# Optimization experiments

Measured on AMD Instinct MI355X. Metric: run time of the kernel, lower is better.

Reference implementation:

```python
import jax, jax.numpy as jnp
import numpy as np

WSZ = 16   # cfg.window_size
GD = 64    # cfg.group_dim


def setup_inputs() -> dict:
    key = jax.random.key(0)
    k1, k2, k3, k4 = jax.random.split(key, 4)
    B, T, D = 8, 8192, 1024
    z = jax.random.normal(k1, (B, T, D), jnp.float32)
    token_lens = jax.random.randint(k2, (B, T), 1, 9).astype(jnp.int32)
    W1 = jax.random.normal(k3, (D, GD), jnp.float32) / np.sqrt(D)
    W2 = jax.random.normal(k4, (GD, GD), jnp.float32) / np.sqrt(GD)
    return {"z": z, "token_lens": token_lens, "W1": W1, "W2": W2, "target_len": 6144}


def _choose_pairs(local_sim, budget):
    # local_sim: (W-1,) sims of adjacent edges inside one window.
    # Greedy non-overlapping matching in descending-sim order, up to `budget` pairs.
    Wn = local_sim.shape[0] + 1
    order = jnp.argsort(-local_sim)

    def step(state, e):
        used, mr, picked = state
        ok = (picked < budget) & (~used[e]) & (~used[e + 1])
        used = used.at[e].set(used[e] | ok)
        used = used.at[e + 1].set(used[e + 1] | ok)
        mr = mr.at[e + 1].set(mr[e + 1] | ok)
        return (used, mr, picked + ok.astype(jnp.int32)), None

    init = (jnp.zeros(Wn, bool), jnp.zeros(Wn, bool), jnp.int32(0))
    (_, mr, _), _ = jax.lax.scan(step, init, order)
    return mr  # (W,) True at j -> merge token j into j-1


def reference(z, token_lens, W1, W2, target_len):
    B, T, D = z.shape
    nwin = T // WSZ  # T chosen divisible by WSZ -> all windows full
    merges_needed = T - target_len
    base, extra = merges_needed // nwin, merges_needed % nwin
    budgets = jnp.minimum(base + (jnp.arange(nwin) < extra), WSZ // 2).astype(jnp.int32)

    # grouping MLP + cosine-style adjacent similarity
    g = jnp.maximum(z @ W1, 0.0) @ W2                         # (B,T,GD)
    g = g / (jnp.linalg.norm(g, axis=-1, keepdims=True) + 1e-8)
    sim = jnp.sum(g[:, :-1] * g[:, 1:], axis=-1)              # (B,T-1)
    # pad boundary edge slot, view per-window; keep only intra-window edges
    sim_pad = jnp.pad(sim, ((0, 0), (0, 1)), constant_values=-jnp.inf)
    local = sim_pad.reshape(B, nwin, WSZ)[:, :, : WSZ - 1]    # (B,nwin,W-1)

    pick = jax.vmap(jax.vmap(_choose_pairs, in_axes=(0, 0)), in_axes=(0, None))
    merge_right = pick(local, budgets).reshape(B, T)          # (B,T) bool
    keep = ~merge_right

    # pairs are disjoint -> sequential torch loop == parallel weighted merge
    w = token_lens.astype(z.dtype)
    absorb = merge_right[:, 1:]                               # token i absorbs i+1
    wi, wj = w[:, :-1, None], w[:, 1:, None]
    merged = (z[:, :-1] * wi + z[:, 1:] * wj) / (wi + wj)
    z2 = jnp.concatenate([jnp.where(absorb[:, :, None], merged, z[:, :-1]), z[:, -1:]], axis=1)
    l2 = jnp.concatenate(
        [jnp.where(absorb, token_lens[:, :-1] + token_lens[:, 1:], token_lens[:, :-1]),
         token_lens[:, -1:]], axis=1)

    # stable compaction: kept indices first (order preserved), truncate
    order = jnp.argsort(~keep, axis=1)[:, :target_len]        # jax sort is stable
    z_new = jnp.take_along_axis(z2, order[:, :, None], axis=1)
    lens_new = jnp.take_along_axis(l2, order, axis=1)
    starts_new = jnp.cumsum(lens_new, axis=1) - lens_new
    return z_new, lens_new, starts_new
```

## Files before the change

### kernel.cpp

```cpp
#include <hip/hip_runtime.h>

#define B_ 8
#define T_ 8192
#define D_ 1024
#define GD_ 64
#define WSZ_ 16
#define NWIN_ (T_ / WSZ_)
#define PL1_ (4 * 32 * 512)
#define PL2_ (4 * 2 * 512)

typedef __attribute__((ext_vector_type(8))) short short8v;
typedef __attribute__((ext_vector_type(4))) float f32x4;

__device__ __forceinline__ unsigned bf16rne(unsigned u) {
  return (u + 0x7FFFu + ((u >> 16) & 1u)) >> 16;
}
__device__ __forceinline__ void split2(float x, short& h, short& m) {
  const unsigned uh = bf16rne(__float_as_uint(x));
  const float fh = __uint_as_float(uh << 16);
  const float r1 = x - fh;
  const unsigned um = bf16rne(__float_as_uint(r1));
  h = (short)uh; m = (short)um;
}

__global__ __launch_bounds__(256) void k_prep(
    const float* __restrict__ W1, const float* __restrict__ W2,
    short* __restrict__ w1f, short* __restrict__ w2f)
{
  const int i = blockIdx.x * 256 + threadIdx.x;
  if (i < 4 * 32 * 64 * 8) {
    const int e = i & 7;
    const int lane = (i >> 3) & 63;
    const int tk = (i >> 9) & 31;
    const int tg = i >> 14;
    const int g = tg * 16 + (lane & 15);
    const int k = tk * 32 + ((lane >> 4) << 3) + e;
    short h, m;
    split2(W1[(long)k * GD_ + g], h, m);
    const int off = ((tg * 32 + tk) << 9) + lane * 8 + e;
    w1f[off] = h;
    w1f[PL1_ + off] = m;
  } else {
    const int j = i - 4 * 32 * 64 * 8;
    const int e = j & 7;
    const int lane = (j >> 3) & 63;
    const int tk = (j >> 9) & 1;
    const int tg = j >> 10;
    const int g = tg * 16 + (lane & 15);
    const int k = tk * 32 + ((lane >> 4) << 3) + e;
    short h, m;
    split2(W2[(long)k * GD_ + g], h, m);
    const int off = ((tg * 2 + tk) << 9) + lane * 8 + e;
    w2f[off] = h;
    w2f[PL2_ + off] = m;
  }
}

__global__ __launch_bounds__(256) void k_fused(
    const float* __restrict__ z, const short* __restrict__ w1f,
    const short* __restrict__ w2f, const int* __restrict__ lensp,
    float* __restrict__ out, double* __restrict__ sims_out,
    int TL, int baseBudget, int doEmit)
{
  __shared__ short Zsp[2][64][72];
  __shared__ double den[64];
  __shared__ double simsL[4][WSZ_ - 1];
  __shared__ int mrmL[4];
  float (*Gf)[72] = (float (*)[72]) & Zsp[0][0][0];

  const int tid = threadIdx.x;
  const int lane = tid & 63;
  const int w = tid >> 6;
  const int th = w & 1;
  const int gh = w >> 1;
  const int cl = lane & 15;
  const int ko8 = (lane >> 4) * 8;
  const long bt0 = (long)blockIdx.x * 64;

  const int r = tid >> 2;
  const int kq = tid & 3;
  const float* zbase = z + (bt0 + r) * D_ + kq * 16;

  f32x4 acc[2][2];
#pragma unroll
  for (int a = 0; a < 2; ++a)
#pragma unroll
    for (int b = 0; b < 2; ++b) acc[a][b] = (f32x4){0.f, 0.f, 0.f, 0.f};

  auto stage = [&](const float4 (&pz)[4]) {
    short h[16], m[16];
#pragma unroll
    for (int q = 0; q < 4; ++q) {
      split2(pz[q].x, h[4 * q + 0], m[4 * q + 0]);
      split2(pz[q].y, h[4 * q + 1], m[4 * q + 1]);
      split2(pz[q].z, h[4 * q + 2], m[4 * q + 2]);
      split2(pz[q].w, h[4 * q + 3], m[4 * q + 3]);
    }
    const int co = kq * 16;
    *(short8v*)&Zsp[0][r][co] =
        (short8v){h[0], h[1], h[2], h[3], h[4], h[5], h[6], h[7]};
    *(short8v*)&Zsp[0][r][co + 8] =
        (short8v){h[8], h[9], h[10], h[11], h[12], h[13], h[14], h[15]};
    *(short8v*)&Zsp[1][r][co] =
        (short8v){m[0], m[1], m[2], m[3], m[4], m[5], m[6], m[7]};
    *(short8v*)&Zsp[1][r][co + 8] =
        (short8v){m[8], m[9], m[10], m[11], m[12], m[13], m[14], m[15]};
  };

  auto mfma_chunk = [&](int c) {
#pragma unroll
    for (int ks = 0; ks < 2; ++ks) {
      const int ko = ks * 32 + ko8;
      short8v af[2][2], bf[2][2];
#pragma unroll
      for (int a = 0; a < 2; ++a)
#pragma unroll
        for (int s = 0; s < 2; ++s)
          af[a][s] = *(const short8v*)(
              w1f + s * PL1_ +
              ((((gh * 2 + a) * 32) + (c * 2 + ks)) << 9) + lane * 8);
#pragma unroll
      for (int b = 0; b < 2; ++b)
#pragma unroll
        for (int s = 0; s < 2; ++s)
          bf[b][s] = *(const short8v*)&Zsp[s][th * 32 + b * 16 + cl][ko];
#pragma unroll
      for (int a = 0; a < 2; ++a)
#pragma unroll
        for (int b = 0; b < 2; ++b) {
          f32x4 d = acc[a][b];
          d = __builtin_amdgcn_mfma_f32_16x16x32_bf16(af[a][0], bf[b][0], d, 0, 0, 0);
          d = __builtin_amdgcn_mfma_f32_16x16x32_bf16(af[a][0], bf[b][1], d, 0, 0, 0);
          d = __builtin_amdgcn_mfma_f32_16x16x32_bf16(af[a][1], bf[b][0], d, 0, 0, 0);
          acc[a][b] = d;
        }
    }
  };

  float4 pzA[4], pzB[4];
#pragma unroll
  for (int q = 0; q < 4; ++q) pzA[q] = *(const float4*)(zbase + 4 * q);

#pragma unroll 1
  for (int c = 0; c < 16; c += 2) {
    if (c) __syncthreads();
    stage(pzA);
    __syncthreads();
#pragma unroll
    for (int q = 0; q < 4; ++q)
      pzB[q] = *(const float4*)(zbase + (c + 1) * 64 + 4 * q);
    mfma_chunk(c);
    __syncthreads();
    stage(pzB);
    __syncthreads();
    if (c + 2 < 16) {
#pragma unroll
      for (int q = 0; q < 4; ++q)
        pzA[q] = *(const float4*)(zbase + (c + 2) * 64 + 4 * q);
    }
    mfma_chunk(c + 1);
  }
  __syncthreads();

#pragma unroll
  for (int a = 0; a < 2; ++a)
#pragma unroll
    for (int b = 0; b < 2; ++b) {
      const int t = th * 32 + b * 16 + cl;
      const int g0 = gh * 32 + a * 16 + (lane >> 4) * 4;
      short hh[4], hm[4];
#pragma unroll
      for (int e = 0; e < 4; ++e)
        split2(fmaxf(acc[a][b][e], 0.0f), hh[e], hm[e]);
      Zsp[0][t][g0 + 0] = hh[0]; Zsp[0][t][g0 + 1] = hh[1];
      Zsp[0][t][g0 + 2] = hh[2]; Zsp[0][t][g0 + 3] = hh[3];
      Zsp[1][t][g0 + 0] = hm[0]; Zsp[1][t][g0 + 1] = hm[1];
      Zsp[1][t][g0 + 2] = hm[2]; Zsp[1][t][g0 + 3] = hm[3];
    }
  __syncthreads();

#pragma unroll
  for (int a = 0; a < 2; ++a)
#pragma unroll
    for (int b = 0; b < 2; ++b) acc[a][b] = (f32x4){0.f, 0.f, 0.f, 0.f};
#pragma unroll
  for (int ks = 0; ks < 2; ++ks) {
    const int ko = ks * 32 + ko8;
    short8v af[2][2], bf[2][2];
#pragma unroll
    for (int a = 0; a < 2; ++a)
#pragma unroll
      for (int s = 0; s < 2; ++s)
        af[a][s] = *(const short8v*)(
            w2f + s * PL2_ + ((((gh * 2 + a) * 2) + ks) << 9) + lane * 8);
#pragma unroll
    for (int b = 0; b < 2; ++b)
#pragma unroll
      for (int s = 0; s < 2; ++s)
        bf[b][s] = *(const short8v*)&Zsp[s][th * 32 + b * 16 + cl][ko];
#pragma unroll
    for (int a = 0; a < 2; ++a)
#pragma unroll
      for (int b = 0; b < 2; ++b) {
        f32x4 d = acc[a][b];
        d = __builtin_amdgcn_mfma_f32_16x16x32_bf16(af[a][0], bf[b][0], d, 0, 0, 0);
        d = __builtin_amdgcn_mfma_f32_16x16x32_bf16(af[a][0], bf[b][1], d, 0, 0, 0);
        d = __builtin_amdgcn_mfma_f32_16x16x32_bf16(af[a][1], bf[b][0], d, 0, 0, 0);
        acc[a][b] = d;
      }
  }
  __syncthreads();

#pragma unroll
  for (int a = 0; a < 2; ++a)
#pragma unroll
    for (int b = 0; b < 2; ++b) {
      const int t = th * 32 + b * 16 + cl;
      const int g0 = gh * 32 + a * 16 + (lane >> 4) * 4;
      *(f32x4*)&Gf[t][g0] = acc[a][b];
    }
  __syncthreads();

  if (tid < 64) {
    double ss = 0.0;
#pragma unroll
    for (int q = 0; q < 16; ++q) {
      const float4 v = *(const float4*)&Gf[tid][4 * q];
      ss += (double)v.x * v.x + (double)v.y * v.y +
            (double)v.z * v.z + (double)v.w * v.w;
    }
    den[tid] = sqrt(ss) + 1e-8;
  }
  __syncthreads();

  if (tid < 4 * (WSZ_ - 1)) {
    const int ww = tid / (WSZ_ - 1), e = tid % (WSZ_ - 1);
    const int t = ww * WSZ_ + e;
    double s = 0.0;
#pragma unroll
    for (int q = 0; q < 16; ++q) {
      const float4 x = *(const float4*)&Gf[t][4 * q];
      const float4 y = *(const float4*)&Gf[t + 1][4 * q];
      s += (double)x.x * y.x + (double)x.y * y.y +
           (double)x.z * y.z + (double)x.w * y.w;
    }
    const double sv = s / (den[t] * den[t + 1]);
    simsL[ww][e] = sv;
    if (!doEmit)
      sims_out[((long)blockIdx.x * 4 + ww) * (WSZ_ - 1) + e] = sv;
  }
  if (!doEmit) return;
  __syncthreads();

  if (tid < 4) {
    double v[WSZ_ - 1];
    int id[WSZ_ - 1];
    for (int e = 0; e < WSZ_ - 1; ++e) { v[e] = simsL[tid][e]; id[e] = e; }
    for (int i = 1; i < WSZ_ - 1; ++i) {
      const double dv = v[i]; const int di = id[i];
      int j = i - 1;
      while (j >= 0 && v[j] < dv) { v[j + 1] = v[j]; id[j + 1] = id[j]; --j; }
      v[j + 1] = dv; id[j + 1] = di;
    }
    bool used[WSZ_];
    for (int i = 0; i < WSZ_; ++i) used[i] = false;
    int mrm = 0, picked = 0;
    for (int ii = 0; ii < WSZ_ - 1; ++ii) {
      const int e = id[ii];
      if (picked < baseBudget && !used[e] && !used[e + 1]) {
        used[e] = used[e + 1] = true;
        mrm |= (1 << (e + 1));
        ++picked;
      }
    }
    mrmL[tid] = mrm;
  }
  __syncthreads();

  const int keptW = WSZ_ - baseBudget;
  const int bb = (int)(bt0 / T_);
  const int tb = (int)(bt0 % T_);
  const int wb = tb / WSZ_;
  const float* zbat = z + (long)bb * T_ * D_;
  const int* lbat = lensp + bb * T_;
  float* lout = out + (long)B_ * TL * D_;

#pragma unroll 1
  for (int ww2 = 0; ww2 < 4; ++ww2) {
    const int mrm = mrmL[ww2];
    int p = keptW * (wb + ww2);
    const int t0 = tb + ww2 * WSZ_;
#pragma unroll 1
    for (int i = 0; i < WSZ_; ++i) {
      if ((mrm >> i) & 1) continue;
      const int t = t0 + i;
      const bool ab = (i < WSZ_ - 1) && ((mrm >> (i + 1)) & 1);
      float4 o = *(const float4*)(zbat + (long)t * D_ + tid * 4);
      if (ab) {
        const float wi = (float)lbat[t], wj = (float)lbat[t + 1];
        const float s = wi + wj;
        const float4 zj = *(const float4*)(zbat + (long)(t + 1) * D_ + tid * 4);
        o.x = (o.x * wi + zj.x * wj) / s;
        o.y = (o.y * wi + zj.y * wj) / s;
        o.z = (o.z * wi + zj.z * wj) / s;
        o.w = (o.w * wi + zj.w * wj) / s;
        if (tid == 0) lout[(long)bb * TL + p] = s;
      } else {
        if (tid == 0) lout[(long)bb * TL + p] = (float)lbat[t];
      }
      *(float4*)(out + ((long)bb * TL + p) * D_ + tid * 4) = o;
      ++p;
    }
  }
}

__global__ __launch_bounds__(64) void k_pick(
    const double* __restrict__ sims, const int* __restrict__ tlptr,
    int* __restrict__ mrMask, int* __restrict__ keptCnt)
{
  const int win = blockIdx.x * 64 + threadIdx.x;
  if (win >= B_ * NWIN_) return;
  const int w = win % NWIN_;
  const int tl = tlptr[0];
  const int mn = T_ - tl;
  const int base = mn / NWIN_, extra = mn % NWIN_;
  int budget = base + (w < extra ? 1 : 0);
  if (budget > WSZ_ / 2) budget = WSZ_ / 2;
  if (budget < 0) budget = 0;
  double v[WSZ_ - 1];
  int id[WSZ_ - 1];
  for (int e = 0; e < WSZ_ - 1; ++e) {
    v[e] = sims[(long)win * (WSZ_ - 1) + e];
    id[e] = e;
  }
  for (int i = 1; i < WSZ_ - 1; ++i) {
    const double dv = v[i]; const int di = id[i];
    int j = i - 1;
    while (j >= 0 && v[j] < dv) { v[j + 1] = v[j]; id[j + 1] = id[j]; --j; }
    v[j + 1] = dv; id[j + 1] = di;
  }
  bool used[WSZ_];
  for (int i = 0; i < WSZ_; ++i) used[i] = false;
  int mrm = 0, picked = 0;
  for (int ii = 0; ii < WSZ_ - 1; ++ii) {
    const int e = id[ii];
    if (picked < budget && !used[e] && !used[e + 1]) {
      used[e] = used[e + 1] = true;
      mrm |= (1 << (e + 1));
      ++picked;
    }
  }
  mrMask[win] = mrm;
  keptCnt[win] = WSZ_ - picked;
}

__global__ void k_scan_windows(const int* __restrict__ keptCnt,
                               int* __restrict__ outOff)
{
  const int b = threadIdx.x;
  if (b >= B_) return;
  int off = 0;
  for (int w = 0; w < NWIN_; ++w) {
    outOff[b * NWIN_ + w] = off;
    off += keptCnt[b * NWIN_ + w];
  }
}

__global__ __launch_bounds__(256) void k_emit(
    const float* __restrict__ z, const int* __restrict__ lens,
    const int* __restrict__ mrMask, const int* __restrict__ outOff,
    float* __restrict__ out, int TL)
{
  const int bw = blockIdx.x;
  const int b = bw / NWIN_, w = bw % NWIN_;
  const int tid = threadIdx.x;
  const int mrm = mrMask[bw];
  int p = outOff[bw];
  const int t0 = w * WSZ_;
  const float* zb = z + (long)b * T_ * D_;
  const int* lb = lens + b * T_;
  float* lout = out + (long)B_ * TL * D_;
  for (int i = 0; i < WSZ_; ++i) {
    if ((mrm >> i) & 1) continue;
    if (p >= TL) return;
    const int t = t0 + i;
    const bool ab = (i < WSZ_ - 1) && ((mrm >> (i + 1)) & 1);
    float4 o = *(const float4*)(zb + (long)t * D_ + tid * 4);
    if (ab) {
      const float wi = (float)lb[t], wj = (float)lb[t + 1];
      const float s = wi + wj;
      const float4 zj = *(const float4*)(zb + (long)(t + 1) * D_ + tid * 4);
      o.x = (o.x * wi + zj.x * wj) / s;
      o.y = (o.y * wi + zj.y * wj) / s;
      o.z = (o.z * wi + zj.z * wj) / s;
      o.w = (o.w * wi + zj.w * wj) / s;
      if (tid == 0) lout[(long)b * TL + p] = s;
    } else {
      if (tid == 0) lout[(long)b * TL + p] = (float)lb[t];
    }
    *(float4*)(out + ((long)b * TL + p) * D_ + tid * 4) = o;
    ++p;
  }
}

__global__ __launch_bounds__(256) void k_starts(
    const float* __restrict__ lens_f, float* __restrict__ starts, int TL)
{
  const int b = blockIdx.x;
  const int tid = threadIdx.x;
  const int lane = tid & 63, wv = tid >> 6;
  __shared__ float wsum[4];
  const float* lrow = lens_f + (long)b * TL;
  float* srow = starts + (long)b * TL;
  float carry = 0.0f;

  for (int c0 = 0; c0 < TL; c0 += 256) {
    const int j = c0 + tid;
    const float v = (j < TL) ? lrow[j] : 0.0f;
    float x = v;
#pragma unroll
    for (int d = 1; d < 64; d <<= 1) {
      const float o = __shfl_up(x, d);
      if (lane >= d) x += o;
    }
    if (lane == 63) wsum[wv] = x;
    __syncthreads();
    float pre = 0.0f;
    if (wv > 0) pre += wsum[0];
    if (wv > 1) pre += wsum[1];
    if (wv > 2) pre += wsum[2];
    const float tot = wsum[0] + wsum[1] + wsum[2] + wsum[3];
    if (j < TL) srow[j] = carry + pre + x - v;
    carry += tot;
    __syncthreads();
  }
}

extern "C" void kernel_launch(void* const* d_in, const int* in_sizes, int n_in,
                              void* d_out, int out_size, void* d_ws, size_t ws_size,
                              hipStream_t stream)
{
  const float* z    = (const float*)d_in[0];
  const int*   lens = (const int*)d_in[1];
  const float* W1   = (const float*)d_in[2];
  const float* W2   = (const float*)d_in[3];
  const int*   tlp  = (const int*)d_in[4];

  float* out = (float*)d_out;
  const int TL = out_size / (B_ * (D_ + 2));

  const int merges = T_ - TL;
  const int base = merges / NWIN_;
  const int extra = merges % NWIN_;
  const int doEmit = (extra == 0 && base >= 0 && base <= 5) ? 1 : 0;

  double* sims = (double*)d_ws;
  char* p = (char*)d_ws + (size_t)B_ * NWIN_ * (WSZ_ - 1) * 8;
  int* mrMask = (int*)p;
  int* kept   = mrMask + B_ * NWIN_;
  int* outOff = kept + B_ * NWIN_;
  short* w1f = (short*)(p + 3 * B_ * NWIN_ * 4 + 64);
  w1f = (short*)(((size_t)w1f + 15) & ~(size_t)15);
  short* w2f = w1f + 2 * PL1_;

  hipLaunchKernelGGL(k_prep,
                     dim3((4 * 32 * 64 * 8 + 4 * 2 * 64 * 8) / 256), dim3(256),
                     0, stream, W1, W2, w1f, w2f);
  hipLaunchKernelGGL(k_fused, dim3((B_ * T_) / 64), dim3(256), 0, stream,
                     z, w1f, w2f, lens, out, sims, TL, base, doEmit);
  if (!doEmit) {
    hipLaunchKernelGGL(k_pick, dim3((B_ * NWIN_ + 63) / 64), dim3(64), 0,
                       stream, sims, tlp, mrMask, kept);
    hipLaunchKernelGGL(k_scan_windows, dim3(1), dim3(64), 0, stream,
                       kept, outOff);
    hipLaunchKernelGGL(k_emit, dim3(B_ * NWIN_), dim3(256), 0, stream,
                       z, lens, mrMask, outOff, out, TL);
  }
  hipLaunchKernelGGL(k_starts, dim3(B_), dim3(256), 0, stream,
                     out + (long)B_ * TL * D_,
                     out + (long)B_ * TL * D_ + (long)B_ * TL, TL);
}
```

Baseline: 186.4 us.

## Double K-chunk size in fused MLP and batch emit loads via precomputed kept list

The GEMM staging loop now handles 128-wide K chunks instead of 64, which halves the number of chunk iterations and the barriers that go with them. The cost is a larger shared buffer and more registers per thread. The emit phase now builds a per-window list of kept tokens with absorb flags ahead of time. It then issues loads for four output rows together before computing and storing them, so global memory latency overlaps across rows. Higher register and LDS use could lower occupancy.

After: 190.1 us. Within noise of the previous version (+2.0%).

```diff
diff --git a/kernel.cpp b/kernel.cpp
--- a/kernel.cpp
+++ b/kernel.cpp
@@ -62,10 +62,11 @@
     float* __restrict__ out, double* __restrict__ sims_out,
     int TL, int baseBudget, int doEmit)
 {
-  __shared__ short Zsp[2][64][72];
+  __shared__ short Zsp[2][64][136];
   __shared__ double den[64];
   __shared__ double simsL[4][WSZ_ - 1];
   __shared__ int mrmL[4];
+  __shared__ int elist[4][WSZ_];
   float (*Gf)[72] = (float (*)[72]) & Zsp[0][0][0];
 
   const int tid = threadIdx.x;
@@ -87,29 +88,41 @@
 #pragma unroll
     for (int b = 0; b < 2; ++b) acc[a][b] = (f32x4){0.f, 0.f, 0.f, 0.f};
 
-  auto stage = [&](const float4 (&pz)[4]) {
-    short h[16], m[16];
-#pragma unroll
-    for (int q = 0; q < 4; ++q) {
-      split2(pz[q].x, h[4 * q + 0], m[4 * q + 0]);
-      split2(pz[q].y, h[4 * q + 1], m[4 * q + 1]);
-      split2(pz[q].z, h[4 * q + 2], m[4 * q + 2]);
-      split2(pz[q].w, h[4 * q + 3], m[4 * q + 3]);
-    }
-    const int co = kq * 16;
-    *(short8v*)&Zsp[0][r][co] =
-        (short8v){h[0], h[1], h[2], h[3], h[4], h[5], h[6], h[7]};
-    *(short8v*)&Zsp[0][r][co + 8] =
-        (short8v){h[8], h[9], h[10], h[11], h[12], h[13], h[14], h[15]};
-    *(short8v*)&Zsp[1][r][co] =
-        (short8v){m[0], m[1], m[2], m[3], m[4], m[5], m[6], m[7]};
-    *(short8v*)&Zsp[1][r][co + 8] =
-        (short8v){m[8], m[9], m[10], m[11], m[12], m[13], m[14], m[15]};
+  auto stageK = [&](const float4 (&pz)[8]) {
+#pragma unroll
+    for (int h2 = 0; h2 < 2; ++h2) {
+      short h[16], m[16];
+#pragma unroll
+      for (int q = 0; q < 4; ++q) {
+        const float4 f = pz[h2 * 4 + q];
+        split2(f.x, h[4 * q + 0], m[4 * q + 0]);
+        split2(f.y, h[4 * q + 1], m[4 * q + 1]);
+        split2(f.z, h[4 * q + 2], m[4 * q + 2]);
+        split2(f.w, h[4 * q + 3], m[4 * q + 3]);
+      }
+      const int co = h2 * 64 + kq * 16;
+      *(short8v*)&Zsp[0][r][co] =
+          (short8v){h[0], h[1], h[2], h[3], h[4], h[5], h[6], h[7]};
+      *(short8v*)&Zsp[0][r][co + 8] =
+          (short8v){h[8], h[9], h[10], h[11], h[12], h[13], h[14], h[15]};
+      *(short8v*)&Zsp[1][r][co] =
+          (short8v){m[0], m[1], m[2], m[3], m[4], m[5], m[6], m[7]};
+      *(short8v*)&Zsp[1][r][co + 8] =
+          (short8v){m[8], m[9], m[10], m[11], m[12], m[13], m[14], m[15]};
+    }
   };
 
+  auto loadPz = [&](float4 (&pz)[8], int c) {
+#pragma unroll
+    for (int q = 0; q < 8; ++q) {
+      const int col = (q >> 2) * 64 + (q & 3) * 4;
+      pz[q] = *(const float4*)(zbase + c * 128 + col);
+    }
+  };
+
   auto mfma_chunk = [&](int c) {
 #pragma unroll
-    for (int ks = 0; ks < 2; ++ks) {
+    for (int ks = 0; ks < 4; ++ks) {
       const int ko = ks * 32 + ko8;
       short8v af[2][2], bf[2][2];
 #pragma unroll
@@ -118,7 +131,7 @@
         for (int s = 0; s < 2; ++s)
           af[a][s] = *(const short8v*)(
               w1f + s * PL1_ +
-              ((((gh * 2 + a) * 32) + (c * 2 + ks)) << 9) + lane * 8);
+              ((((gh * 2 + a) * 32) + (c * 4 + ks)) << 9) + lane * 8);
 #pragma unroll
       for (int b = 0; b < 2; ++b)
 #pragma unroll
@@ -137,27 +150,20 @@
     }
   };
 
-  float4 pzA[4], pzB[4];
-#pragma unroll
-  for (int q = 0; q < 4; ++q) pzA[q] = *(const float4*)(zbase + 4 * q);
+  float4 pzA[8], pzB[8];
+  loadPz(pzA, 0);
 
 #pragma unroll 1
-  for (int c = 0; c < 16; c += 2) {
+  for (int c = 0; c < 8; c += 2) {
     if (c) __syncthreads();
-    stage(pzA);
+    stageK(pzA);
     __syncthreads();
-#pragma unroll
-    for (int q = 0; q < 4; ++q)
-      pzB[q] = *(const float4*)(zbase + (c + 1) * 64 + 4 * q);
+    loadPz(pzB, c + 1);
     mfma_chunk(c);
     __syncthreads();
-    stage(pzB);
+    stageK(pzB);
     __syncthreads();
-    if (c + 2 < 16) {
-#pragma unroll
-      for (int q = 0; q < 4; ++q)
-        pzA[q] = *(const float4*)(zbase + (c + 2) * 64 + 4 * q);
-    }
+    if (c + 2 < 8) loadPz(pzA, c + 2);
     mfma_chunk(c + 1);
   }
   __syncthreads();
@@ -274,6 +280,12 @@
       }
     }
     mrmL[tid] = mrm;
+    int cnt = 0;
+    for (int i = 0; i < WSZ_; ++i) {
+      if ((mrm >> i) & 1) continue;
+      const bool ab = (i < WSZ_ - 1) && ((mrm >> (i + 1)) & 1);
+      elist[tid][cnt++] = i | (ab ? 256 : 0);
+    }
   }
   __syncthreads();
 
@@ -287,29 +299,45 @@
 
 #pragma unroll 1
   for (int ww2 = 0; ww2 < 4; ++ww2) {
-    const int mrm = mrmL[ww2];
-    int p = keptW * (wb + ww2);
+    const int pbase = keptW * (wb + ww2);
     const int t0 = tb + ww2 * WSZ_;
 #pragma unroll 1
-    for (int i = 0; i < WSZ_; ++i) {
-      if ((mrm >> i) & 1) continue;
-      const int t = t0 + i;
-      const bool ab = (i < WSZ_ - 1) && ((mrm >> (i + 1)) & 1);
-      float4 o = *(const float4*)(zbat + (long)t * D_ + tid * 4);
-      if (ab) {
-        const float wi = (float)lbat[t], wj = (float)lbat[t + 1];
-        const float s = wi + wj;
-        const float4 zj = *(const float4*)(zbat + (long)(t + 1) * D_ + tid * 4);
-        o.x = (o.x * wi + zj.x * wj) / s;
-        o.y = (o.y * wi + zj.y * wj) / s;
-        o.z = (o.z * wi + zj.z * wj) / s;
-        o.w = (o.w * wi + zj.w * wj) / s;
-        if (tid == 0) lout[(long)bb * TL + p] = s;
-      } else {
-        if (tid == 0) lout[(long)bb * TL + p] = (float)lbat[t];
+    for (int j0 = 0; j0 < keptW; j0 += 4) {
+      float4 oi[4], oj[4];
+      int ti[4];
+      bool ab[4], vl[4];
+#pragma unroll
+      for (int jj = 0; jj < 4; ++jj) {
+        const int j = j0 + jj;
+        vl[jj] = (j < keptW);
+        if (vl[jj]) {
+          const int e = elist[ww2][j];
+          ab[jj] = (e >> 8) != 0;
+          const int t = t0 + (e & 255);
+          ti[jj] = t;
+          oi[jj] = *(const float4*)(zbat + (long)t * D_ + tid * 4);
+          if (ab[jj])
+            oj[jj] = *(const float4*)(zbat + (long)(t + 1) * D_ + tid * 4);
+        }
       }
-      *(float4*)(out + ((long)bb * TL + p) * D_ + tid * 4) = o;
-      ++p;
+#pragma unroll
+      for (int jj = 0; jj < 4; ++jj) {
+        if (!vl[jj]) continue;
+        const int p = pbase + j0 + jj;
+        float4 o = oi[jj];
+        if (ab[jj]) {
+          const float wi = (float)lbat[ti[jj]], wj2 = (float)lbat[ti[jj] + 1];
+          const float s = wi + wj2;
+          o.x = (o.x * wi + oj[jj].x * wj2) / s;
+          o.y = (o.y * wi + oj[jj].y * wj2) / s;
+          o.z = (o.z * wi + oj[jj].z * wj2) / s;
+          o.w = (o.w * wi + oj[jj].w * wj2) / s;
+          if (tid == 0) lout[(long)bb * TL + p] = s;
+        } else {
+          if (tid == 0) lout[(long)bb * TL + p] = (float)lbat[ti[jj]];
+        }
+        *(float4*)(out + ((long)bb * TL + p) * D_ + tid * 4) = o;
+      }
     }
   }
 }
```
